# Performance work log

Hardware: AMD Instinct MI355X
Metric: run time of the kernel (lower is better)

The kernel has to match this reference:

```python
import jax, jax.numpy as jnp
import numpy as np

B, T, D, W, H = 8, 2048, 1024, 16, 8
HD = D // H  # head dim = 128
EPS = 1e-5


def _layernorm(x, g, b):
    m = jnp.mean(x, axis=-1, keepdims=True)
    v = jnp.var(x, axis=-1, keepdims=True)
    return (x - m) / jnp.sqrt(v + EPS) * g + b


def setup_inputs() -> dict:
    key = jax.random.key(0)
    ks = jax.random.split(key, 8)
    s = 0.02
    return {
        "frame_features": jax.random.normal(ks[0], (B, T, D), dtype=jnp.float32),
        "frame_indices": jnp.arange(B * T, dtype=jnp.int64).reshape(B, T),
        # nn.MultiheadAttention packed in-projection (3D, D) and out projection
        "w_qkv": jax.random.normal(ks[1], (3 * D, D), dtype=jnp.float32) * s,
        "b_qkv": jnp.zeros((3 * D,), dtype=jnp.float32),
        "w_out": jax.random.normal(ks[2], (D, D), dtype=jnp.float32) * s,
        "b_out": jnp.zeros((D,), dtype=jnp.float32),
        # FFN: Linear(D, 4D) -> GELU -> Linear(4D, D)
        "w1": jax.random.normal(ks[3], (4 * D, D), dtype=jnp.float32) * s,
        "b1": jnp.zeros((4 * D,), dtype=jnp.float32),
        "w2": jax.random.normal(ks[4], (D, 4 * D), dtype=jnp.float32) * s,
        "b2": jnp.zeros((D,), dtype=jnp.float32),
        "g1": jnp.ones((D,), dtype=jnp.float32),
        "beta1": jnp.zeros((D,), dtype=jnp.float32),
        "g2": jnp.ones((D,), dtype=jnp.float32),
        "beta2": jnp.zeros((D,), dtype=jnp.float32),
    }


def _forward(frame_features, frame_indices, w_qkv, b_qkv, w_out, b_out,
             w1, b1, w2, b2, g1, beta1, g2, beta2):
    # --- sinusoidal temporal positional encoding, indexed by frame number ---
    pos = frame_indices.astype(jnp.float32)[..., None]          # (B, T, 1)
    div = jnp.exp(-jnp.log(10000.0) * jnp.arange(0, D, 2, dtype=jnp.float32) / D)
    ang = pos * div                                              # (B, T, D/2)
    pe = jnp.stack([jnp.sin(ang), jnp.cos(ang)], axis=-1).reshape(B, T, D)
    x = frame_features + pe

    # --- block-diagonal (local window) attention, all windows in one pass ---
    nw = T // W
    xw = x.reshape(B, nw, W, D)
    qkv = jnp.einsum('bnwd,ed->bnwe', xw, w_qkv) + b_qkv         # (B, nw, W, 3D)
    q, k, v = jnp.split(qkv, 3, axis=-1)
    q = q.reshape(B, nw, W, H, HD)
    k = k.reshape(B, nw, W, H, HD)
    v = v.reshape(B, nw, W, H, HD)
    scores = jnp.einsum('bnqhd,bnkhd->bnhqk', q, k) / jnp.sqrt(jnp.float32(HD))
    attn = jax.nn.softmax(scores, axis=-1)
    o = jnp.einsum('bnhqk,bnkhd->bnqhd', attn, v).reshape(B, nw, W, D)
    attn_out = jnp.einsum('bnwd,ed->bnwe', o, w_out) + b_out

    h = _layernorm(xw + attn_out, g1, beta1)
    ffn = jnp.einsum('bnwf,df->bnwd', jax.nn.gelu(
        jnp.einsum('bnwd,fd->bnwf', h, w1) + b1, approximate=False), w2) + b2
    out = _layernorm(h + ffn, g2, beta2)
    return out.reshape(B, T, D)


def reference(frame_features, frame_indices, w_qkv, b_qkv, w_out, b_out,
              w1, b1, w2, b2, g1, beta1, g2, beta2):
    return _forward(frame_features, frame_indices, w_qkv, b_qkv, w_out, b_out,
                    w1, b1, w2, b2, g1, beta1, g2, beta2)
```

## Files before the change

### kernel.cpp

```cpp
#include <hip/hip_runtime.h>
#include <math.h>

typedef __bf16 bf16;
typedef __bf16 bf16x8 __attribute__((ext_vector_type(8)));
typedef __bf16 bf16x4 __attribute__((ext_vector_type(4)));
typedef __bf16 bf16x2 __attribute__((ext_vector_type(2)));
typedef float f32x4 __attribute__((ext_vector_type(4)));

#define ROWS 16384
#define DD   1024

typedef __attribute__((address_space(3))) void* lds_vp;
typedef const __attribute__((address_space(1))) void* glb_vp;
__device__ __forceinline__ void gload16(const void* g, void* l) {
  __builtin_amdgcn_global_load_lds((glb_vp)g, (lds_vp)l, 16, 0, 0);
}

__global__ __launch_bounds__(256) void cast_kernel(
    const float* __restrict__ src, bf16* __restrict__ dst, int n)
{
  int i = (blockIdx.x * 256 + threadIdx.x) * 8;
  if (i >= n) return;
  float4 a = *(const float4*)(src + i);
  float4 b = *(const float4*)(src + i + 4);
  bf16x8 o;
  o[0] = (bf16)a.x; o[1] = (bf16)a.y; o[2] = (bf16)a.z; o[3] = (bf16)a.w;
  o[4] = (bf16)b.x; o[5] = (bf16)b.y; o[6] = (bf16)b.z; o[7] = (bf16)b.w;
  *(bf16x8*)(dst + i) = o;
}

__global__ __launch_bounds__(256) void pe_add_kernel(
    const float* __restrict__ ff, const int* __restrict__ idx, bf16* __restrict__ x)
{
  int p   = blockIdx.x * 256 + threadIdx.x;
  int row = p >> 9;
  int j   = p & 511;
  float pos = (float)idx[row];
  float d2  = (float)(2 * j) * (1.0f / 1024.0f);
  float dv  = expf(-9.210340371976184f * d2);
  float ang = pos * dv;
  float s, c;
  sincosf(ang, &s, &c);
  int base = row * 1024 + 2 * j;
  float2 f = *(const float2*)(ff + base);
  bf16x2 o;
  o[0] = (bf16)(f.x + s);
  o[1] = (bf16)(f.y + c);
  *(bf16x2*)(x + base) = o;
}

template<bool GELU, bool RES>
__global__ __launch_bounds__(256, 2) void gemm_bt(
    const bf16* __restrict__ A, const bf16* __restrict__ Bw,
    const float* __restrict__ bias, const bf16* __restrict__ resid,
    bf16* __restrict__ C, int M, int N, int K)
{
  __shared__ bf16 smem[8192];
  bf16* sA = smem;
  bf16* sB = smem + 4096;

  const int tid = threadIdx.x;

  int lid = blockIdx.y * gridDim.x + blockIdx.x;
  int xcd = lid & 7;
  int j   = lid >> 3;
  const int bm = (xcd * 16 + (j & 15)) * 128;
  const int bn = (j >> 4) * 128;

  const int wave = tid >> 6;
  const int lane = tid & 63;
  const int wr   = (wave >> 1) * 64;
  const int wc   = (wave & 1) * 64;
  const int ln   = lane & 15;
  const int q    = lane >> 4;

  const int srow = lane >> 2;
  const int sgr  = (((lane & 3) ^ ((lane >> 3) & 3))) * 8;

  const int slot = (q ^ ((ln >> 1) & 3)) * 8;

  f32x4 acc[4][4];
#pragma unroll
  for (int i = 0; i < 4; i++)
#pragma unroll
    for (int jj = 0; jj < 4; jj++) acc[i][jj] = {0.f, 0.f, 0.f, 0.f};

  const bf16* ga0 = A  + (size_t)(bm + wave * 16 + srow) * K + sgr;
  const bf16* ga1 = A  + (size_t)(bm + (wave + 4) * 16 + srow) * K + sgr;
  const bf16* gb0 = Bw + (size_t)(bn + wave * 16 + srow) * K + sgr;
  const bf16* gb1 = Bw + (size_t)(bn + (wave + 4) * 16 + srow) * K + sgr;
  bf16* la0 = &sA[(wave * 16) * 32];
  bf16* la1 = &sA[((wave + 4) * 16) * 32];
  bf16* lb0 = &sB[(wave * 16) * 32];
  bf16* lb1 = &sB[((wave + 4) * 16) * 32];

  for (int k0 = 0; k0 < K; k0 += 32) {
    __syncthreads();
    gload16(ga0 + k0, la0);
    gload16(ga1 + k0, la1);
    gload16(gb0 + k0, lb0);
    gload16(gb1 + k0, lb1);
    __syncthreads();

    bf16x8 af[4], bfr[4];
#pragma unroll
    for (int t = 0; t < 4; t++) {
      af[t]  = *(const bf16x8*)(&sA[(wr + t * 16 + ln) * 32 + slot]);
      bfr[t] = *(const bf16x8*)(&sB[(wc + t * 16 + ln) * 32 + slot]);
    }
#pragma unroll
    for (int tm = 0; tm < 4; tm++)
#pragma unroll
      for (int tn = 0; tn < 4; tn++)
        acc[tm][tn] = __builtin_amdgcn_mfma_f32_16x16x32_bf16(
            af[tm], bfr[tn], acc[tm][tn], 0, 0, 0);
  }

  const int lr_w = (wave >> 1) * 16 + q * 4;
  const int lr_r = tid >> 3;
  const int cb   = (tid & 7) * 16;
#pragma unroll
  for (int tm = 0; tm < 4; tm++) {
    __syncthreads();
#pragma unroll
    for (int tn = 0; tn < 4; tn++) {
      int gn = bn + wc + tn * 16 + ln;
      float bv = bias[gn];
#pragma unroll
      for (int i = 0; i < 4; i++)
        smem[(lr_w + i) * 132 + wc + tn * 16 + ln] = (bf16)(acc[tm][tn][i] + bv);
    }
    __syncthreads();
    int gR = bm + (lr_r >> 4) * 64 + tm * 16 + (lr_r & 15);
    size_t rowoff = (size_t)gR * N + bn + cb;
    bf16x8 v0 = *(const bf16x8*)&smem[lr_r * 132 + cb];
    bf16x8 v1 = *(const bf16x8*)&smem[lr_r * 132 + cb + 8];
    if (RES) {
      bf16x8 r0 = *(const bf16x8*)(resid + rowoff);
      bf16x8 r1 = *(const bf16x8*)(resid + rowoff + 8);
#pragma unroll
      for (int u = 0; u < 8; u++) {
        v0[u] = (bf16)((float)v0[u] + (float)r0[u]);
        v1[u] = (bf16)((float)v1[u] + (float)r1[u]);
      }
    }
    if (GELU) {
#pragma unroll
      for (int u = 0; u < 8; u++) {
        float a = (float)v0[u], b = (float)v1[u];
        v0[u] = (bf16)(0.5f * a * (1.0f + erff(a * 0.70710678118654752f)));
        v1[u] = (bf16)(0.5f * b * (1.0f + erff(b * 0.70710678118654752f)));
      }
    }
    *(bf16x8*)(C + rowoff)     = v0;
    *(bf16x8*)(C + rowoff + 8) = v1;
  }
}

__global__ __launch_bounds__(256) void attn_kernel(
    const bf16* __restrict__ qkv, bf16* __restrict__ o)
{
  __shared__ float sq[16][132], sk[16][132], sv[16][132];
  __shared__ float ss[16][17];

  int wid = blockIdx.x;
  int h   = wid & 7;
  int win = wid >> 3;
  int tb  = win * 16;

  int t  = threadIdx.x;
  int r  = t >> 4;
  int c8 = (t & 15) * 8;

  const bf16* base = qkv + (size_t)(tb + r) * 3072 + c8;
  bf16x8 qv = *(const bf16x8*)(base + h * 128);
  bf16x8 kv = *(const bf16x8*)(base + 1024 + h * 128);
  bf16x8 vv = *(const bf16x8*)(base + 2048 + h * 128);
#pragma unroll
  for (int u = 0; u < 8; u++) {
    sq[r][c8 + u] = (float)qv[u];
    sk[r][c8 + u] = (float)kv[u];
    sv[r][c8 + u] = (float)vv[u];
  }
  __syncthreads();

  {
    int i = t >> 4, jj = t & 15;
    float s = 0.f;
#pragma unroll 8
    for (int d = 0; d < 128; d++) s += sq[i][d] * sk[jj][d];
    ss[i][jj] = s * 0.08838834764831845f;
  }
  __syncthreads();

  if (t < 16) {
    float m = -1e30f;
    for (int jj = 0; jj < 16; jj++) m = fmaxf(m, ss[t][jj]);
    float sum = 0.f;
    for (int jj = 0; jj < 16; jj++) { float e = expf(ss[t][jj] - m); ss[t][jj] = e; sum += e; }
    float inv = 1.0f / sum;
    for (int jj = 0; jj < 16; jj++) ss[t][jj] *= inv;
  }
  __syncthreads();

  {
    int i = t >> 4; int d0 = (t & 15) * 8;
    float acc[8] = {0, 0, 0, 0, 0, 0, 0, 0};
#pragma unroll
    for (int jj = 0; jj < 16; jj++) {
      float a = ss[i][jj];
#pragma unroll
      for (int u = 0; u < 8; u++) acc[u] += a * sv[jj][d0 + u];
    }
    bf16* op = o + (size_t)(tb + i) * 1024 + h * 128 + d0;
#pragma unroll
    for (int u = 0; u < 8; u++) op[u] = (bf16)acc[u];
  }
}

template<typename OUT_T>
__global__ __launch_bounds__(256) void ln_kernel(
    const bf16* __restrict__ x, const float* __restrict__ g,
    const float* __restrict__ b, OUT_T* __restrict__ y)
{
  __shared__ float red[8];
  int row = blockIdx.x;
  int t   = threadIdx.x;
  int lane = t & 63, wave = t >> 6;

  bf16x4 v4 = *(const bf16x4*)(x + (size_t)row * 1024 + t * 4);
  float v[4];
  float s = 0.f, sq = 0.f;
#pragma unroll
  for (int u = 0; u < 4; u++) {
    v[u] = (float)v4[u];
    s += v[u];
    sq += v[u] * v[u];
  }
  for (int off = 32; off > 0; off >>= 1) {
    s  += __shfl_down(s, off);
    sq += __shfl_down(sq, off);
  }
  if (lane == 0) { red[wave * 2] = s; red[wave * 2 + 1] = sq; }
  __syncthreads();
  float st = red[0] + red[2] + red[4] + red[6];
  float qt = red[1] + red[3] + red[5] + red[7];
  float mean = st * (1.0f / 1024.0f);
  float var  = qt * (1.0f / 1024.0f) - mean * mean;
  float inv  = rsqrtf(var + 1e-5f);
  int c = t * 4;
  OUT_T* yr = y + (size_t)row * 1024 + c;
#pragma unroll
  for (int u = 0; u < 4; u++)
    yr[u] = (OUT_T)((v[u] - mean) * inv * g[c + u] + b[c + u]);
}

extern "C" void kernel_launch(void* const* d_in, const int* in_sizes, int n_in,
                              void* d_out, int out_size, void* d_ws, size_t ws_size,
                              hipStream_t stream) {
  const float* ff    = (const float*)d_in[0];
  const int*   idx   = (const int*)d_in[1];
  const float* w_qkv = (const float*)d_in[2];
  const float* b_qkv = (const float*)d_in[3];
  const float* w_out = (const float*)d_in[4];
  const float* b_out = (const float*)d_in[5];
  const float* w1    = (const float*)d_in[6];
  const float* b1    = (const float*)d_in[7];
  const float* w2    = (const float*)d_in[8];
  const float* b2    = (const float*)d_in[9];
  const float* g1    = (const float*)d_in[10];
  const float* be1   = (const float*)d_in[11];
  const float* g2    = (const float*)d_in[12];
  const float* be2   = (const float*)d_in[13];
  float* out = (float*)d_out;

  char* p = (char*)d_ws;
  bf16* x_bf = (bf16*)p;  p += (size_t)ROWS * 1024 * 2;
  bf16* big  = (bf16*)p;  p += (size_t)ROWS * 4096 * 2;
  bf16* s_bf = (bf16*)p;  p += (size_t)ROWS * 1024 * 2;
  bf16* h_bf = (bf16*)p;  p += (size_t)ROWS * 1024 * 2;
  bf16* wqb  = (bf16*)p;  p += (size_t)3072 * 1024 * 2;
  bf16* wob  = (bf16*)p;  p += (size_t)1024 * 1024 * 2;
  bf16* w1b  = (bf16*)p;  p += (size_t)4096 * 1024 * 2;
  bf16* w2b  = (bf16*)p;  p += (size_t)1024 * 4096 * 2;
  bf16* o_bf = big + (size_t)ROWS * 3072;
  bf16* g_bf = big;

  cast_kernel<<<3072 * 1024 / 8 / 256, 256, 0, stream>>>(w_qkv, wqb, 3072 * 1024);
  cast_kernel<<<1024 * 1024 / 8 / 256, 256, 0, stream>>>(w_out, wob, 1024 * 1024);
  cast_kernel<<<4096 * 1024 / 8 / 256, 256, 0, stream>>>(w1, w1b, 4096 * 1024);
  cast_kernel<<<1024 * 4096 / 8 / 256, 256, 0, stream>>>(w2, w2b, 1024 * 4096);

  pe_add_kernel<<<ROWS * 512 / 256, 256, 0, stream>>>(ff, idx, x_bf);
  gemm_bt<false, false><<<dim3(3072 / 128, ROWS / 128), 256, 0, stream>>>(
      x_bf, wqb, b_qkv, nullptr, big, ROWS, 3072, 1024);
  attn_kernel<<<(ROWS / 16) * 8, 256, 0, stream>>>(big, o_bf);
  gemm_bt<false, true><<<dim3(1024 / 128, ROWS / 128), 256, 0, stream>>>(
      o_bf, wob, b_out, x_bf, s_bf, ROWS, 1024, 1024);
  ln_kernel<bf16><<<ROWS, 256, 0, stream>>>(s_bf, g1, be1, h_bf);
  gemm_bt<true, false><<<dim3(4096 / 128, ROWS / 128), 256, 0, stream>>>(
      h_bf, w1b, b1, nullptr, g_bf, ROWS, 4096, 1024);
  gemm_bt<false, true><<<dim3(1024 / 128, ROWS / 128), 256, 0, stream>>>(
      g_bf, w2b, b2, h_bf, s_bf, ROWS, 1024, 4096);
  ln_kernel<float><<<ROWS, 256, 0, stream>>>(s_bf, g2, be2, out);
}
```

Baseline: 747.1 us.

## Replace direct global-to-LDS loads with register-prefetched staging and remap tile order

The GEMM mainloop stops using global_load_lds and instead loads the next K-slice into registers before the barrier, then writes the current slice into LDS with a new XOR swizzle. This overlaps global latency with the MFMA work of the current iteration, at the cost of extra VGPRs and explicit LDS store instructions. The block-to-tile mapping also changes, from grouping M tiles per XCD to spreading N tiles across XCDs, which alters L2 reuse of the weight and activation tiles.

```diff
diff --git a/kernel.cpp b/kernel.cpp
--- a/kernel.cpp
+++ b/kernel.cpp
@@ -8,13 +8,6 @@
 typedef float f32x4 __attribute__((ext_vector_type(4)));
 
 #define ROWS 16384
-#define DD   1024
-
-typedef __attribute__((address_space(3))) void* lds_vp;
-typedef const __attribute__((address_space(1))) void* glb_vp;
-__device__ __forceinline__ void gload16(const void* g, void* l) {
-  __builtin_amdgcn_global_load_lds((glb_vp)g, (lds_vp)l, 16, 0, 0);
-}
 
 __global__ __launch_bounds__(256) void cast_kernel(
     const float* __restrict__ src, bf16* __restrict__ dst, int n)
@@ -62,10 +55,11 @@
   const int tid = threadIdx.x;
 
   int lid = blockIdx.y * gridDim.x + blockIdx.x;
-  int xcd = lid & 7;
-  int j   = lid >> 3;
-  const int bm = (xcd * 16 + (j & 15)) * 128;
-  const int bn = (j >> 4) * 128;
+  int per = gridDim.x >> 3;
+  int s   = lid & 7;
+  int t_  = lid >> 3;
+  const int bn = (s * per + (t_ % per)) * 128;
+  const int bm = (t_ / per) * 128;
 
   const int wave = tid >> 6;
   const int lane = tid & 63;
@@ -74,10 +68,10 @@
   const int ln   = lane & 15;
   const int q    = lane >> 4;
 
-  const int srow = lane >> 2;
-  const int sgr  = (((lane & 3) ^ ((lane >> 3) & 3))) * 8;
-
-  const int slot = (q ^ ((ln >> 1) & 3)) * 8;
+  const int sr = tid >> 2;
+  const int sg = tid & 3;
+  const int p0 = (sg ^ (sr & 3)) * 8;
+  const int slot = (q ^ (ln & 3)) * 8;
 
   f32x4 acc[4][4];
 #pragma unroll
@@ -85,21 +79,29 @@
 #pragma unroll
     for (int jj = 0; jj < 4; jj++) acc[i][jj] = {0.f, 0.f, 0.f, 0.f};
 
-  const bf16* ga0 = A  + (size_t)(bm + wave * 16 + srow) * K + sgr;
-  const bf16* ga1 = A  + (size_t)(bm + (wave + 4) * 16 + srow) * K + sgr;
-  const bf16* gb0 = Bw + (size_t)(bn + wave * 16 + srow) * K + sgr;
-  const bf16* gb1 = Bw + (size_t)(bn + (wave + 4) * 16 + srow) * K + sgr;
-  bf16* la0 = &sA[(wave * 16) * 32];
-  bf16* la1 = &sA[((wave + 4) * 16) * 32];
-  bf16* lb0 = &sB[(wave * 16) * 32];
-  bf16* lb1 = &sB[((wave + 4) * 16) * 32];
+  const bf16* pa0 = A  + (size_t)(bm + sr)      * K + sg * 8;
+  const bf16* pa1 = A  + (size_t)(bm + sr + 64) * K + sg * 8;
+  const bf16* pb0 = Bw + (size_t)(bn + sr)      * K + sg * 8;
+  const bf16* pb1 = Bw + (size_t)(bn + sr + 64) * K + sg * 8;
+
+  float4 a0 = *(const float4*)(pa0);
+  float4 a1 = *(const float4*)(pa1);
+  float4 b0 = *(const float4*)(pb0);
+  float4 b1 = *(const float4*)(pb1);
 
   for (int k0 = 0; k0 < K; k0 += 32) {
+    float4 na0, na1, nb0, nb1;
+    if (k0 + 32 < K) {
+      na0 = *(const float4*)(pa0 + k0 + 32);
+      na1 = *(const float4*)(pa1 + k0 + 32);
+      nb0 = *(const float4*)(pb0 + k0 + 32);
+      nb1 = *(const float4*)(pb1 + k0 + 32);
+    }
     __syncthreads();
-    gload16(ga0 + k0, la0);
-    gload16(ga1 + k0, la1);
-    gload16(gb0 + k0, lb0);
-    gload16(gb1 + k0, lb1);
+    *(float4*)(&sA[sr * 32 + p0])        = a0;
+    *(float4*)(&sA[(sr + 64) * 32 + p0]) = a1;
+    *(float4*)(&sB[sr * 32 + p0])        = b0;
+    *(float4*)(&sB[(sr + 64) * 32 + p0]) = b1;
     __syncthreads();
 
     bf16x8 af[4], bfr[4];
@@ -114,6 +116,8 @@
       for (int tn = 0; tn < 4; tn++)
         acc[tm][tn] = __builtin_amdgcn_mfma_f32_16x16x32_bf16(
             af[tm], bfr[tn], acc[tm][tn], 0, 0, 0);
+
+    a0 = na0; a1 = na1; b0 = nb0; b1 = nb1;
   }
 
   const int lr_w = (wave >> 1) * 16 + q * 4;
```

Result: slower. 831.8 us (+11.3%).
